# Optimization experiments

Hardware: AMD Instinct MI355X
Metric: run time of the kernel (lower is better)

The kernel has to match this reference:

```python
import jax, jax.numpy as jnp
import numpy as np

NUM_PROJS = 8
BLOCK = 128      # key_block_size; with n=4096 -> 32 blocks, query_block_size=128 too
SAMPLE = 128     # sample_size
HEAD_DIM = 64
SCALE = HEAD_DIM ** -0.5

def _gray_perm(n):
    # AngularLSH._unit_hamming_distance_array: Gray-code ordering of 2^n sign buckets
    a = np.array([0, 1], dtype=np.int32)
    for _ in range(n - 1):
        a = np.concatenate([a, a[::-1] + a.shape[0]])
    return a

PERM = jnp.asarray(_gray_perm(NUM_PROJS))
ENC = jnp.asarray(2 ** np.arange(NUM_PROJS), dtype=jnp.int32)

def _lsh_hash(x, proj_dir):
    # x: [b,h,n,d], proj_dir: [d,r] -> Gray-coded bucket id [b,h,n]
    bits = (jnp.einsum('bhnd,dr->bhnr', x, proj_dir) > 0).astype(jnp.int32)
    return PERM[jnp.sum(bits * ENC, axis=-1)]

def _gather_seq(x, idx):
    # gather along seq axis (axis=2); idx: [b,h,m]
    return jnp.take_along_axis(x, idx[..., None], axis=2)

def _hyper_attention(q, k, v, proj_dir, sampled_set):
    # q,k,v: [b,h,n,d]; non-causal HyperAttention (n >= min_seq_len path)
    b, h, n, d = q.shape
    # --- 1. sortLSH block-diagonal attention ---
    q_idx = jnp.argsort(_lsh_hash(q, proj_dir), axis=2, stable=True)
    k_idx = jnp.argsort(_lsh_hash(k, proj_dir), axis=2, stable=True)
    q_idx_inv = jnp.argsort(q_idx, axis=2, stable=True)
    qs = _gather_seq(q, q_idx)
    ks = _gather_seq(k, k_idx)
    vs = _gather_seq(v, k_idx)
    nb = n // BLOCK
    qb = qs.reshape(b, h, nb, BLOCK, d)
    kb = ks.reshape(b, h, nb, BLOCK, d)
    vb = vs.reshape(b, h, nb, BLOCK, d)
    s = jnp.einsum('bhgqd,bhgkd->bhgqk', qb, kb) * SCALE
    lse_blk = jax.scipy.special.logsumexp(s, axis=-1).reshape(b, h, n)
    attn_blk = jnp.einsum('bhgqk,bhgkd->bhgqd', jax.nn.softmax(s, axis=-1), vb).reshape(b, h, n, d)
    # --- 2. uniformly sampled residual (low-rank correction) ---
    ksub = _gather_seq(ks, sampled_set)   # [b,h,m,d]
    vsub = _gather_seq(vs, sampled_set)
    row_blk = jnp.arange(n) // BLOCK       # query_block_size == BLOCK here
    mask = row_blk[None, None, :, None] == (sampled_set // BLOCK)[:, :, None, :]
    bias = jnp.where(mask, jnp.finfo(q.dtype).min, jnp.zeros((), q.dtype))
    sr = jnp.einsum('bhnd,bhmd->bhnm', qs, ksub) * SCALE + bias
    lse_res = jax.scipy.special.logsumexp(sr, axis=-1) + jnp.log(jnp.asarray(n / SAMPLE, q.dtype))
    attn_res = jnp.einsum('bhnm,bhmd->bhnd', jax.nn.softmax(sr, axis=-1), vsub)
    # --- combine the two attention estimates (add_self_attentions) ---
    lse = jnp.logaddexp(lse_blk, lse_res)
    w1 = jnp.exp(lse_blk - lse)[..., None]
    attn = w1 * attn_blk + (1.0 - w1) * attn_res
    # --- unsort rows back to original query order ---
    return _gather_seq(attn, q_idx_inv)

def setup_inputs() -> dict:
    key = jax.random.key(0)
    k1, k2, k3 = jax.random.split(key, 3)
    qkv = jax.random.normal(k1, (2, 4096, 3, 16, 64), dtype=jnp.float32)
    proj_dir = jax.random.normal(k2, (64, NUM_PROJS), dtype=jnp.float32)
    sampled_set = jax.random.randint(k3, (2, 16, SAMPLE), 0, 4096)
    return {"qkv": qkv, "proj_dir": proj_dir, "sampled_set": sampled_set}

def reference(qkv, proj_dir, sampled_set):
    # qkv: [B,S,3,H,D] -> q,k,v [B,H,S,D]
    q = jnp.transpose(qkv[:, :, 0], (0, 2, 1, 3))
    k = jnp.transpose(qkv[:, :, 1], (0, 2, 1, 3))
    v = jnp.transpose(qkv[:, :, 2], (0, 2, 1, 3))
    out = _hyper_attention(q, k, v, proj_dir, sampled_set)
    return jnp.transpose(out, (0, 2, 1, 3))  # [B,S,H,D]
```

## Files before the change

kernel.cpp:

```cpp
#include <hip/hip_runtime.h>
#include <hip/hip_bf16.h>

#define NSEQ 4096
#define NBH 32
#define LOG32 3.4657359028f
#define QSCALE 0.125f

typedef unsigned short us8 __attribute__((ext_vector_type(8)));
typedef __bf16 bf16x8 __attribute__((ext_vector_type(8)));
typedef float f32x4 __attribute__((ext_vector_type(4)));
typedef unsigned int u32x4 __attribute__((ext_vector_type(4)));

__device__ __forceinline__ unsigned short f2b(float x) {
    __bf16 h = (__bf16)x;
    return __builtin_bit_cast(unsigned short, h);
}
__device__ __forceinline__ unsigned pk2(float lo, float hi) {
    return (unsigned)f2b(lo) | ((unsigned)f2b(hi) << 16);
}
__device__ __forceinline__ bf16x8 cvt8(float4 a, float4 b) {
    us8 u;
    u[0] = f2b(a.x); u[1] = f2b(a.y); u[2] = f2b(a.z); u[3] = f2b(a.w);
    u[4] = f2b(b.x); u[5] = f2b(b.y); u[6] = f2b(b.z); u[7] = f2b(b.w);
    return __builtin_bit_cast(bf16x8, u);
}

__global__ __launch_bounds__(256) void hash_kernel(const float* __restrict__ qkv,
                                                   const float* __restrict__ proj,
                                                   unsigned short* __restrict__ hsh) {
    __shared__ float pdT[512];
    int tid = threadIdx.x;
    for (int j = tid; j < 512; j += 256) pdT[j] = proj[(j & 63) * 8 + (j >> 6)];
    __syncthreads();
    int j0 = blockIdx.x * 256 + tid;
    #pragma unroll
    for (int rep = 0; rep < 2; ++rep) {
        int j = j0 + rep * 131072;
        int ch = rep;
        int bh = (j >> 12) & 31;
        int i = j & 4095;
        int b = bh >> 4, h = bh & 15;
        const float4* src = (const float4*)(qkv + ((size_t)((b * NSEQ + i) * 3 + ch)) * 1024 + h * 64);
        double acc[8] = {0, 0, 0, 0, 0, 0, 0, 0};
        for (int d4 = 0; d4 < 16; ++d4) {
            float4 x = src[d4];
            double xx = x.x, xy = x.y, xz = x.z, xw = x.w;
            #pragma unroll
            for (int r = 0; r < 8; ++r) {
                const float4 p = *(const float4*)&pdT[r * 64 + d4 * 4];
                acc[r] += xx * p.x + xy * p.y + xz * p.z + xw * p.w;
            }
        }
        int c = 0;
        #pragma unroll
        for (int r = 0; r < 8; ++r)
            if (acc[r] > 0.0) c |= (1 << r);
        hsh[j] = (unsigned short)(c ^ (c >> 1));
    }
}

__global__ __launch_bounds__(1024) void sort_kernel(const unsigned short* __restrict__ hsh,
                                                    int* __restrict__ qidx,
                                                    int* __restrict__ kidx) {
    int blk = blockIdx.x;
    int pass = blk >> 5, bh = blk & 31;
    const unsigned short* src = hsh + pass * 131072 + bh * 4096;
    int* outg = (pass ? kidx : qidx) + bh * 4096;
    int tid = threadIdx.x;
    __shared__ unsigned short hl[4096];
    __shared__ int hist[64][256];
    __shared__ int base[256];
    for (int j = tid; j < 64 * 256; j += 1024) (&hist[0][0])[j] = 0;
    __syncthreads();
    for (int j = tid; j < 4096; j += 1024) {
        unsigned short v = src[j];
        hl[j] = v;
        atomicAdd(&hist[j >> 6][v], 1);
    }
    __syncthreads();
    int cnt_tot = 0;
    if (tid < 256) {
        int tot = 0;
        #pragma unroll
        for (int s = 0; s < 64; ++s) { int c = hist[s][tid]; hist[s][tid] = tot; tot += c; }
        base[tid] = tot;
        cnt_tot = tot;
    }
    __syncthreads();
    for (int off = 1; off < 256; off <<= 1) {
        int t = (tid >= off && tid < 256) ? base[tid - off] : 0;
        __syncthreads();
        if (tid >= off && tid < 256) base[tid] += t;
        __syncthreads();
    }
    int incl = 0;
    if (tid < 256) incl = base[tid];
    __syncthreads();
    if (tid < 256) base[tid] = incl - cnt_tot;
    __syncthreads();
    {
        int seg = tid >> 4, cls = tid & 15;
        for (int ii = 0; ii < 64; ++ii) {
            int i = (seg << 6) + ii;
            int q = hl[i];
            if ((q & 15) == cls) {
                int pos = base[q] + hist[seg][q];
                hist[seg][q] = hist[seg][q] + 1;
                outg[pos] = i;
            }
        }
    }
}

__global__ __launch_bounds__(512, 4) void attn_kernel(const float* __restrict__ qkv,
                                                      const int* __restrict__ sampled,
                                                      const int* __restrict__ qidx_g,
                                                      const int* __restrict__ kidx_g,
                                                      float* __restrict__ out) {
    int bid = blockIdx.x;
    int gb = (bid & 7) * 128 + (bid >> 3);
    int bh = gb >> 5, g = gb & 31;
    int b = bh >> 4, h = bh & 15;
    int tid = threadIdx.x;
    int w = tid >> 6, l = tid & 63;
    int l15 = l & 15, lq = l >> 4;

    __shared__ us8 KP[2048];
    __shared__ us8 VT[2048];
    __shared__ float colbias[256];

    const int* qbase_g = qidx_g + bh * NSEQ + g * 128;
    const int* kbase_g = kidx_g + bh * NSEQ + g * 128;
    const int* smp = sampled + bh * 128;

    if (tid < 128) {
        colbias[tid] = 0.0f;
    } else if (tid < 256) {
        int sp = smp[tid - 128];
        colbias[tid] = ((sp >> 7) == g) ? -1e30f : LOG32;
    }

    int qr = qbase_g[w * 16 + l15];
    const float* qbase = qkv + ((size_t)((b * NSEQ + qr) * 3 + 0)) * 1024 + h * 64 + lq * 8;
    float4 qa0 = *(const float4*)(qbase);
    float4 qa1 = *(const float4*)(qbase + 4);
    float4 qb0 = *(const float4*)(qbase + 32);
    float4 qb1 = *(const float4*)(qbase + 36);

    {
        int r0 = tid >> 2, qt = tid & 3;
        int r1 = r0 + 128;
        int kr0 = kbase_g[r0];
        int sp0 = smp[r0];
        int kr1 = kidx_g[bh * NSEQ + sp0];
        const float4* src0 = (const float4*)(qkv + ((size_t)((b * NSEQ + kr0) * 3 + 1)) * 1024 + h * 64 + qt * 16);
        const float4* src1 = (const float4*)(qkv + ((size_t)((b * NSEQ + kr1) * 3 + 1)) * 1024 + h * 64 + qt * 16);
        float4 k0 = src0[0], k1 = src0[1], k2 = src0[2], k3 = src0[3];
        float4 k4 = src1[0], k5 = src1[1], k6 = src1[2], k7 = src1[3];
        int sw0 = (r0 ^ (r0 >> 2)) & 7;
        int sw1 = (r1 ^ (r1 >> 2)) & 7;
        KP[r0 * 8 + ((qt * 2) ^ sw0)]     = __builtin_bit_cast(us8, cvt8(k0, k1));
        KP[r0 * 8 + ((qt * 2 + 1) ^ sw0)] = __builtin_bit_cast(us8, cvt8(k2, k3));
        KP[r1 * 8 + ((qt * 2) ^ sw1)]     = __builtin_bit_cast(us8, cvt8(k4, k5));
        KP[r1 * 8 + ((qt * 2 + 1) ^ sw1)] = __builtin_bit_cast(us8, cvt8(k6, k7));
    }
    {
        int vkey = tid >> 1, vhalf = tid & 1;
        int vr = (vkey < 128) ? kbase_g[vkey] : kidx_g[bh * NSEQ + smp[vkey - 128]];
        const float4* src = (const float4*)(qkv + ((size_t)((b * NSEQ + vr) * 3 + 2)) * 1024 + h * 64 + vhalf * 32);
        unsigned short* vt_us = (unsigned short*)VT;
        int kc8 = vkey >> 3, ke = vkey & 7;
        #pragma unroll
        for (int d4 = 0; d4 < 8; ++d4) {
            float4 f = src[d4];
            int d = vhalf * 32 + d4 * 4;
            vt_us[(((d + 0) * 32 + (kc8 ^ ((d + 0) & 7))) << 3) + ke] = f2b(f.x);
            vt_us[(((d + 1) * 32 + (kc8 ^ ((d + 1) & 7))) << 3) + ke] = f2b(f.y);
            vt_us[(((d + 2) * 32 + (kc8 ^ ((d + 2) & 7))) << 3) + ke] = f2b(f.z);
            vt_us[(((d + 3) * 32 + (kc8 ^ ((d + 3) & 7))) << 3) + ke] = f2b(f.w);
        }
    }
    __syncthreads();

    bf16x8 q0 = cvt8(qa0, qa1);
    bf16x8 q1 = cvt8(qb0, qb1);
    f32x4 sA[8], sB[8];
    int ra = 8 * (l15 >> 2) + (l15 & 3);
    #pragma unroll
    for (int s = 0; s < 8; ++s) {
        int krA = s * 32 + ra;
        int krB = krA + 4;
        int swA = (krA ^ (krA >> 2)) & 7;
        int swB = (krB ^ (krB >> 2)) & 7;
        bf16x8 kA0 = __builtin_bit_cast(bf16x8, KP[krA * 8 + (lq ^ swA)]);
        bf16x8 kA1 = __builtin_bit_cast(bf16x8, KP[krA * 8 + ((lq + 4) ^ swA)]);
        bf16x8 kB0 = __builtin_bit_cast(bf16x8, KP[krB * 8 + (lq ^ swB)]);
        bf16x8 kB1 = __builtin_bit_cast(bf16x8, KP[krB * 8 + ((lq + 4) ^ swB)]);
        f32x4 accA = {0.f, 0.f, 0.f, 0.f}, accB = {0.f, 0.f, 0.f, 0.f};
        accA = __builtin_amdgcn_mfma_f32_16x16x32_bf16(kA0, q0, accA, 0, 0, 0);
        accA = __builtin_amdgcn_mfma_f32_16x16x32_bf16(kA1, q1, accA, 0, 0, 0);
        accB = __builtin_amdgcn_mfma_f32_16x16x32_bf16(kB0, q0, accB, 0, 0, 0);
        accB = __builtin_amdgcn_mfma_f32_16x16x32_bf16(kB1, q1, accB, 0, 0, 0);
        float4 cbA = *(const float4*)&colbias[s * 32 + lq * 8];
        float4 cbB = *(const float4*)&colbias[s * 32 + lq * 8 + 4];
        sA[s][0] = accA[0] * QSCALE + cbA.x;
        sA[s][1] = accA[1] * QSCALE + cbA.y;
        sA[s][2] = accA[2] * QSCALE + cbA.z;
        sA[s][3] = accA[3] * QSCALE + cbA.w;
        sB[s][0] = accB[0] * QSCALE + cbB.x;
        sB[s][1] = accB[1] * QSCALE + cbB.y;
        sB[s][2] = accB[2] * QSCALE + cbB.z;
        sB[s][3] = accB[3] * QSCALE + cbB.w;
    }

    float m = -1e30f;
    #pragma unroll
    for (int s = 0; s < 8; ++s)
        #pragma unroll
        for (int j = 0; j < 4; ++j) {
            m = fmaxf(m, sA[s][j]);
            m = fmaxf(m, sB[s][j]);
        }
    m = fmaxf(m, __shfl_xor(m, 16));
    m = fmaxf(m, __shfl_xor(m, 32));
    float sum = 0.f;
    #pragma unroll
    for (int s = 0; s < 8; ++s)
        #pragma unroll
        for (int j = 0; j < 4; ++j) {
            float pa = __expf(sA[s][j] - m); sA[s][j] = pa; sum += pa;
            float pb = __expf(sB[s][j] - m); sB[s][j] = pb; sum += pb;
        }
    sum += __shfl_xor(sum, 16);
    sum += __shfl_xor(sum, 32);
    float rs = 1.0f / sum;

    int4 qr4 = *(const int4*)&qbase_g[w * 16 + lq * 4];

    f32x4 oacc[4] = {{0.f,0.f,0.f,0.f},{0.f,0.f,0.f,0.f},{0.f,0.f,0.f,0.f},{0.f,0.f,0.f,0.f}};
    #pragma unroll
    for (int s = 0; s < 8; ++s) {
        u32x4 pw;
        pw[0] = pk2(sA[s][0] * rs, sA[s][1] * rs);
        pw[1] = pk2(sA[s][2] * rs, sA[s][3] * rs);
        pw[2] = pk2(sB[s][0] * rs, sB[s][1] * rs);
        pw[3] = pk2(sB[s][2] * rs, sB[s][3] * rs);
        bf16x8 pa = __builtin_bit_cast(bf16x8, pw);
        #pragma unroll
        for (int ct = 0; ct < 4; ++ct) {
            int d = ct * 16 + l15;
            bf16x8 vb = __builtin_bit_cast(bf16x8, VT[d * 32 + ((s * 4 + lq) ^ (d & 7))]);
            oacc[ct] = __builtin_amdgcn_mfma_f32_16x16x32_bf16(pa, vb, oacc[ct], 0, 0, 0);
        }
    }

    int qrows[4] = {qr4.x, qr4.y, qr4.z, qr4.w};
    #pragma unroll
    for (int j = 0; j < 4; ++j) {
        size_t obase = ((size_t)((b * NSEQ + qrows[j]) * 16 + h)) * 64;
        #pragma unroll
        for (int ct = 0; ct < 4; ++ct)
            out[obase + ct * 16 + l15] = oacc[ct][j];
    }
}

extern "C" void kernel_launch(void* const* d_in, const int* in_sizes, int n_in,
                              void* d_out, int out_size, void* d_ws, size_t ws_size,
                              hipStream_t stream) {
    const float* qkv = (const float*)d_in[0];
    const float* proj = (const float*)d_in[1];
    const int* sampled = (const int*)d_in[2];
    float* outp = (float*)d_out;

    int* qidx = (int*)d_ws;
    int* kidx = qidx + NBH * NSEQ;
    unsigned short* hsh = (unsigned short*)(kidx + NBH * NSEQ);

    hash_kernel<<<512, 256, 0, stream>>>(qkv, proj, hsh);
    sort_kernel<<<64, 1024, 0, stream>>>(hsh, qidx, kidx);
    attn_kernel<<<NBH * 32, 512, 0, stream>>>(qkv, sampled, qidx, kidx, outp);
}
```

Measured before the change: 74.09 us.

## Replace serial sort scatter with wave-ballot match ranking for stable counting sort

The counting sort now computes each element's stable rank within its 64-element segment using eight wave ballots that match equal bucket ids. This replaces per-element shared atomics and the 64-iteration serial scatter loop. The histogram is written by the first lane of each bucket group, and the final scatter becomes fully parallel across threads. It adds ballot work per element and byte-sized shared arrays, and correctness depends on the wavefront size being 64 to match the segment size.

```diff
diff --git a/kernel.cpp b/kernel.cpp
--- a/kernel.cpp
+++ b/kernel.cpp
@@ -67,21 +67,32 @@
     const unsigned short* src = hsh + pass * 131072 + bh * 4096;
     int* outg = (pass ? kidx : qidx) + bh * 4096;
     int tid = threadIdx.x;
-    __shared__ unsigned short hl[4096];
+    int wv = tid >> 6, ln = tid & 63;
     __shared__ int hist[64][256];
+    __shared__ unsigned char rnk[4096];
+    __shared__ unsigned char bkt[4096];
     __shared__ int base[256];
-    for (int j = tid; j < 64 * 256; j += 1024) (&hist[0][0])[j] = 0;
-    __syncthreads();
-    for (int j = tid; j < 4096; j += 1024) {
-        unsigned short v = src[j];
-        hl[j] = v;
-        atomicAdd(&hist[j >> 6][v], 1);
+    for (int jj = tid; jj < 64 * 256; jj += 1024) (&hist[0][0])[jj] = 0;
+    __syncthreads();
+    for (int s = wv; s < 64; s += 16) {
+        int i = s * 64 + ln;
+        int q = src[i];
+        bkt[i] = (unsigned char)q;
+        unsigned long long mask = ~0ULL;
+        #pragma unroll
+        for (int bit = 0; bit < 8; ++bit) {
+            unsigned long long bb = __ballot((q >> bit) & 1);
+            mask &= ((q >> bit) & 1) ? bb : ~bb;
+        }
+        int r = __popcll(mask & ((1ULL << ln) - 1ULL));
+        rnk[i] = (unsigned char)r;
+        if (r == 0) hist[s][q] = __popcll(mask);
     }
     __syncthreads();
     int cnt_tot = 0;
     if (tid < 256) {
         int tot = 0;
-        #pragma unroll
+        #pragma unroll 8
         for (int s = 0; s < 64; ++s) { int c = hist[s][tid]; hist[s][tid] = tot; tot += c; }
         base[tid] = tot;
         cnt_tot = tot;
@@ -98,17 +109,9 @@
     __syncthreads();
     if (tid < 256) base[tid] = incl - cnt_tot;
     __syncthreads();
-    {
-        int seg = tid >> 4, cls = tid & 15;
-        for (int ii = 0; ii < 64; ++ii) {
-            int i = (seg << 6) + ii;
-            int q = hl[i];
-            if ((q & 15) == cls) {
-                int pos = base[q] + hist[seg][q];
-                hist[seg][q] = hist[seg][q] + 1;
-                outg[pos] = i;
-            }
-        }
+    for (int i = tid; i < 4096; i += 1024) {
+        int q = bkt[i];
+        outg[base[q] + hist[i >> 6][q] + rnk[i]] = i;
     }
 }
 
```

Measured after the change: 69.51 us. 6.2% less time.
